# Kernel optimization log

Measured on AMD Instinct MI355X. Metric: run time of the kernel, lower is better.

The kernel has to match this reference:

```python
import jax, jax.numpy as jnp
import numpy as np

B, N, D = 8, 1024, 1024
H, HD = 16, 64          # n_heads, head_dim = D // H
FF = 2 * D              # SwiGLU hidden dim (ffn_dim_mult=2)
EPS = 1e-5


def setup_inputs() -> dict:
    key = jax.random.key(0)
    ks = jax.random.split(key, 10)
    s = 0.02
    return {
        "x": jax.random.normal(ks[0], (B, N, D), dtype=jnp.float32),
        "attn_norm_scale": jnp.ones((D,), jnp.float32),
        "ffn_norm_scale": jnp.ones((D,), jnp.float32),
        "wq": jax.random.normal(ks[1], (D, D), jnp.float32) * s,
        "bq": jnp.zeros((D,), jnp.float32),
        "wk": jax.random.normal(ks[2], (D, D), jnp.float32) * s,
        "bk": jnp.zeros((D,), jnp.float32),
        "wv": jax.random.normal(ks[3], (D, D), jnp.float32) * s,
        "bv": jnp.zeros((D,), jnp.float32),
        "wo": jax.random.normal(ks[4], (D, D), jnp.float32) * s,
        "bo": jnp.zeros((D,), jnp.float32),
        "w_uv": jax.random.normal(ks[5], (D, 2 * FF), jnp.float32) * s,
        "w_out": jax.random.normal(ks[6], (FF, D), jnp.float32) * s,
    }


def _rmsnorm(x, scale):
    xf = x.astype(jnp.float32)
    y = xf * jax.lax.rsqrt(jnp.mean(xf * xf, axis=-1, keepdims=True) + EPS)
    return scale * y.astype(x.dtype)


def reference(x, attn_norm_scale, ffn_norm_scale, wq, bq, wk, bk, wv, bv,
              wo, bo, w_uv, w_out):
    # FFT2D: fft over channel dim then token dim, keep real part
    x = jnp.fft.fft(jnp.fft.fft(x, axis=-1), axis=-2).real.astype(jnp.float32)

    # --- self attention with pre-RMSNorm and residual ---
    xn = _rmsnorm(x, attn_norm_scale)
    q = (xn @ wq + bq).reshape(B, N, H, HD)
    k = (xn @ wk + bk).reshape(B, N, H, HD)
    v = (xn @ wv + bv).reshape(B, N, H, HD)
    scores = jnp.einsum('bnhd,bmhd->bhnm', q, k) / np.sqrt(HD).astype(np.float32)
    attn = jax.nn.softmax(scores, axis=-1)
    o = jnp.einsum('bhnm,bmhd->bnhd', attn, v).reshape(B, N, D)
    x = (o @ wo + bo) + x

    # --- SwiGLU FFN with pre-RMSNorm and residual ---
    xn = _rmsnorm(x, ffn_norm_scale)
    uv = xn @ w_uv                      # [B, N, 2*FF]
    u, vg = uv[..., :FF], uv[..., FF:]
    x = (jax.nn.silu(u) * vg) @ w_out + x
    return x
```

## Files before the change

kernel.cpp:

```cpp
#include <hip/hip_runtime.h>
#include <stdint.h>

typedef unsigned short u16;
typedef __attribute__((ext_vector_type(8))) __bf16 bf16x8;
typedef __attribute__((ext_vector_type(4))) float f32x4;
typedef __attribute__((ext_vector_type(8))) u16 u16x8;

static __device__ __forceinline__ u16 f2bf(float f){
  uint32_t x = __builtin_bit_cast(uint32_t, f);
  x = (x + 0x7FFFu + ((x >> 16) & 1u)) >> 16;
  return (u16)x;
}
static __device__ __forceinline__ u16 f2bf_fast(float f){
  uint32_t x = __builtin_bit_cast(uint32_t, f);
  return (u16)((x + 0x8000u) >> 16);
}
static __device__ __forceinline__ float bf2f(u16 h){
  uint32_t x = ((uint32_t)h) << 16;
  return __builtin_bit_cast(float, x);
}
static __device__ __forceinline__ f32x4 mfma16(bf16x8 a, bf16x8 b, f32x4 c){
  return __builtin_amdgcn_mfma_f32_16x16x32_bf16(a, b, c, 0, 0, 0);
}
static __device__ __forceinline__ void gload16(const void* g, void* l){
  __builtin_amdgcn_global_load_lds(
      (const __attribute__((address_space(1))) void*)(uintptr_t)g,
      (__attribute__((address_space(3))) void*)(uint32_t)(uintptr_t)l,
      16, 0, 0);
}

__global__ __launch_bounds__(256) void k_prep(
    const float* __restrict__ x,  const float* __restrict__ wq,
    const float* __restrict__ wk, const float* __restrict__ wv,
    const float* __restrict__ wo, const float* __restrict__ wuv,
    const float* __restrict__ wout,
    const float* __restrict__ bq, const float* __restrict__ bk,
    const float* __restrict__ bv,
    u16* __restrict__ Cb, u16* __restrict__ Sb, u16* __restrict__ xbt,
    u16* __restrict__ wqkvt, u16* __restrict__ wot, u16* __restrict__ wuvt,
    u16* __restrict__ woutt, float* __restrict__ bqkv)
{
  int bid = blockIdx.x;
  int t = threadIdx.x;
  if (bid < 1024){
    int n = bid, m0 = t * 4;
    #pragma unroll
    for (int i = 0; i < 4; ++i){
      int m = m0 + i;
      int ph = (n * m) & 1023;
      float a = (float)ph * (1.0f / 512.0f);
      int idx = n * 1024 + m;
      Cb[idx] = f2bf(cospif(a)); Sb[idx] = f2bf(sinpif(a));
    }
    return;
  }
  bid -= 1024;
  if (bid >= 18432){
    int i = (bid - 18432) * 256 + t;
    bqkv[i] = i < 1024 ? bq[i] : (i < 2048 ? bk[i - 1024] : bv[i - 2048]);
    return;
  }
  __shared__ float tl[32][33];
  const float* in; u16* out; int Cc, R, bx, by;
  int64_t inOff = 0, outOff = 0;
  bool uvperm = false;
  if (bid < 8192){
    int z = bid >> 10, tile = bid & 1023;
    in = x; out = xbt; Cc = 1024; R = 1024;
    inOff = (int64_t)z << 20; outOff = (int64_t)z << 20;
    bx = tile & 31; by = tile >> 5;
  } else if (bid < 12288){
    int j = (bid - 8192) >> 10, tile = (bid - 8192) & 1023;
    const float* srcs[4] = {wq, wk, wv, wo};
    in = srcs[j]; Cc = 1024; R = 1024;
    if (j < 3){ out = wqkvt; outOff = (int64_t)j << 20; }
    else      { out = wot; }
    bx = tile & 31; by = tile >> 5;
  } else if (bid < 16384){
    int tile = bid - 12288;
    in = wuv; out = wuvt; Cc = 4096; R = 1024; uvperm = true;
    bx = tile & 127; by = tile >> 7;
  } else {
    int tile = bid - 16384;
    in = wout; out = woutt; Cc = 1024; R = 2048;
    bx = tile & 31; by = tile >> 6;
    by = tile >> 5;
  }
  int tc = bx * 32, tr = by * 32;
  int lx = t & 31, ly = t >> 5;
  const float* ip = in + inOff;
  #pragma unroll
  for (int i = 0; i < 32; i += 8)
    tl[ly + i][lx] = ip[(int64_t)(tr + ly + i) * Cc + tc + lx];
  __syncthreads();
  if (uvperm){
    #pragma unroll
    for (int i = 0; i < 32; i += 8){
      int c = tc + ly + i;
      int pr = (c < 2048) ? ((c >> 4) * 32 + (c & 15))
                          : (((c - 2048) >> 4) * 32 + 16 + ((c - 2048) & 15));
      out[(int64_t)pr * 1024 + tr + lx] = f2bf(tl[lx][ly + i]);
    }
  } else {
    u16* op = out + outOff;
    #pragma unroll
    for (int i = 0; i < 32; i += 8)
      op[(int64_t)(tc + ly + i) * R + tr + lx] = f2bf(tl[lx][ly + i]);
  }
}

__global__ __launch_bounds__(256) void k_rmsnorm(const float* __restrict__ x,
                                                 const float* __restrict__ sc,
                                                 u16* __restrict__ out){
  int r = blockIdx.x;
  const float4* px = (const float4*)(x + (int64_t)r * 1024);
  float4 v = px[threadIdx.x];
  float ss = v.x*v.x + v.y*v.y + v.z*v.z + v.w*v.w;
  #pragma unroll
  for (int o = 1; o < 64; o <<= 1) ss += __shfl_xor(ss, o);
  __shared__ float red[4];
  if ((threadIdx.x & 63) == 0) red[threadIdx.x >> 6] = ss;
  __syncthreads();
  float tot = red[0] + red[1] + red[2] + red[3];
  float rs = rsqrtf(tot * (1.0f / 1024.0f) + 1e-5f);
  float4 s4 = ((const float4*)sc)[threadIdx.x];
  ushort4 ov;
  ov.x = f2bf(v.x * rs * s4.x); ov.y = f2bf(v.y * rs * s4.y);
  ov.z = f2bf(v.z * rs * s4.z); ov.w = f2bf(v.w * rs * s4.w);
  ((ushort4*)(out + (int64_t)r * 1024))[threadIdx.x] = ov;
}

__global__ __launch_bounds__(256) void k_fftfin(const u16* __restrict__ Uw,
                                                const float* __restrict__ sc,
                                                float* __restrict__ Y,
                                                u16* __restrict__ xn){
  int row = blockIdx.x;
  int b = row >> 10, k = row & 1023;
  int kp = (k <= 512) ? k : 1024 - k;
  float sgn = (k <= 512) ? -1.0f : 1.0f;
  const u16* ub = Uw + (int64_t)b * (1280 * 1024) + (int64_t)kp * 1024;
  const u16* wb = ub + 640 * 1024;
  int c4 = threadIdx.x * 4;
  ushort4 uu = *(const ushort4*)(ub + c4);
  ushort4 ww = *(const ushort4*)(wb + c4);
  float y0 = bf2f(uu.x) + sgn * bf2f(ww.x);
  float y1 = bf2f(uu.y) + sgn * bf2f(ww.y);
  float y2 = bf2f(uu.z) + sgn * bf2f(ww.z);
  float y3 = bf2f(uu.w) + sgn * bf2f(ww.w);
  float ss = y0*y0 + y1*y1 + y2*y2 + y3*y3;
  #pragma unroll
  for (int o = 1; o < 64; o <<= 1) ss += __shfl_xor(ss, o);
  __shared__ float red[4];
  if ((threadIdx.x & 63) == 0) red[threadIdx.x >> 6] = ss;
  __syncthreads();
  float tot = red[0] + red[1] + red[2] + red[3];
  float rs = rsqrtf(tot * (1.0f / 1024.0f) + 1e-5f);
  float4 s4 = ((const float4*)sc)[threadIdx.x];
  float4 yo; yo.x = y0; yo.y = y1; yo.z = y2; yo.w = y3;
  ((float4*)(Y + (int64_t)row * 1024))[threadIdx.x] = yo;
  ushort4 ov;
  ov.x = f2bf(y0 * rs * s4.x); ov.y = f2bf(y1 * rs * s4.y);
  ov.z = f2bf(y2 * rs * s4.z); ov.w = f2bf(y3 * rs * s4.w);
  ((ushort4*)(xn + (int64_t)row * 1024))[threadIdx.x] = ov;
}

template<bool SILU>
__global__ __launch_bounds__(256, 4) void k_gemm4(
    const u16* __restrict__ A0, const u16* __restrict__ A1,
    const u16* __restrict__ B0, const u16* __restrict__ B1,
    void* Cout, const float* __restrict__ bias, const float* resid,
    int nkt, int rowSplit, int lda, int ldb, int ldc,
    int64_t aB, int64_t bB, int64_t cB, int outBf16)
{
  __shared__ char smem[32768];

  int z = blockIdx.z;
  int nwg = gridDim.x * gridDim.y;
  int bid = blockIdx.y * gridDim.x + blockIdx.x;
  int sw = (bid & 7) * (nwg >> 3) + (bid >> 3);
  int bx = sw % gridDim.x, by = sw / gridDim.x;

  int tm = by * 128, tn = bx * 128;
  int tid = threadIdx.x;
  int lane = tid & 63, w = tid >> 6;
  int lr = lane & 15, lg = lane >> 4;
  int wOffM = (w >> 1) * 64, wOffN = (w & 1) * 64;

  const u16* Ap = ((tm < rowSplit) ? A0 : A1) + (int64_t)z * aB;
  const u16* Bp = ((tm < rowSplit) ? B0 : B1) + (int64_t)z * bB;
  int64_t cOff = (int64_t)z * cB;

  int r0_, kg0_, r1_, kg1_;
  {
    int D = tid * 16, line = D >> 7, sp = ((D >> 4) & 7) ^ (line & 7);
    r0_ = line * 2 + (sp >> 2); kg0_ = sp & 3;
    D = tid * 16 + 4096; line = D >> 7; sp = ((D >> 4) & 7) ^ (line & 7);
    r1_ = line * 2 + (sp >> 2); kg1_ = sp & 3;
  }
  const u16* pA0 = Ap + (int64_t)(tm + r0_) * lda + kg0_ * 8;
  const u16* pA1 = Ap + (int64_t)(tm + r1_) * lda + kg1_ * 8;
  const u16* pB0 = Bp + (int64_t)(tn + r0_) * ldb + kg0_ * 8;
  const u16* pB1 = Bp + (int64_t)(tn + r1_) * ldb + kg1_ * 8;

  int slotR = (lg + ((lr & 1) << 2)) ^ ((lr >> 1) & 7);
  int aRB = ((wOffM >> 1) + (lr >> 1)) * 128 + slotR * 16;
  int bRB = ((wOffN >> 1) + (lr >> 1)) * 128 + slotR * 16;

  const f32x4 fz = {0.f, 0.f, 0.f, 0.f};
  f32x4 acc[4][4];
  #pragma unroll
  for (int i = 0; i < 4; ++i)
    #pragma unroll
    for (int j = 0; j < 4; ++j) acc[i][j] = fz;

  auto STAGE = [&](int kt, int bf){
    int k0 = kt * 32;
    char* d = smem + bf * 16384 + tid * 16;
    gload16(pA0 + k0, d);
    gload16(pA1 + k0, d + 4096);
    gload16(pB0 + k0, d + 8192);
    gload16(pB1 + k0, d + 12288);
  };
  auto COMPUTE = [&](const char* Ab){
    const char* Bb = Ab + 8192;
    bf16x8 af[4], bfr[4];
    #pragma unroll
    for (int i = 0; i < 4; ++i) af[i]  = *(const bf16x8*)(Ab + aRB + i * 1024);
    #pragma unroll
    for (int j = 0; j < 4; ++j) bfr[j] = *(const bf16x8*)(Bb + bRB + j * 1024);
    #pragma unroll
    for (int i = 0; i < 4; ++i)
      #pragma unroll
      for (int j = 0; j < 4; ++j)
        acc[i][j] = mfma16(af[i], bfr[j], acc[i][j]);
  };

  STAGE(0, 0);
  __syncthreads();
  for (int kt = 0; kt < nkt; kt += 2){
    STAGE(kt + 1, 1);
    COMPUTE(smem);
    __syncthreads();
    if (kt + 2 < nkt) STAGE(kt + 2, 0);
    COMPUTE(smem + 16384);
    __syncthreads();
  }

  if constexpr (SILU){
    int colBase = ((tn + wOffN) >> 1) + lr;
    #pragma unroll
    for (int i = 0; i < 4; ++i){
      #pragma unroll
      for (int jj = 0; jj < 4; ++jj){
        int row = tm + wOffM + i * 16 + lg * 4 + jj;
        #pragma unroll
        for (int jp = 0; jp < 2; ++jp){
          float u = acc[i][jp * 2][jj], v = acc[i][jp * 2 + 1][jj];
          float s = u / (1.0f + __expf(-u));
          ((u16*)Cout)[(int64_t)row * ldc + colBase + jp * 16] = f2bf(s * v);
        }
      }
    }
  } else {
    #pragma unroll
    for (int i = 0; i < 4; ++i){
      #pragma unroll
      for (int j = 0; j < 4; ++j){
        int col = tn + wOffN + j * 16 + lr;
        float badd = bias ? bias[col] : 0.0f;
        #pragma unroll
        for (int jj = 0; jj < 4; ++jj){
          int row = tm + wOffM + i * 16 + lg * 4 + jj;
          int64_t idx = cOff + (int64_t)row * ldc + col;
          float v = acc[i][j][jj] + badd;
          if (resid) v += resid[idx];
          if (outBf16) ((u16*)Cout)[idx] = f2bf(v);
          else         ((float*)Cout)[idx] = v;
        }
      }
    }
  }
}

__global__ __launch_bounds__(256) void k_vtrans(const u16* __restrict__ qkv,
                                                u16* __restrict__ vt){
  __shared__ u16 T[64 * 65];
  int bh = blockIdx.y; int b = bh >> 4, h = bh & 15;
  int kt = blockIdx.x;
  int t = threadIdx.x;
  const u16* src = qkv + (int64_t)(b * 1024 + kt * 64) * 3072 + 2048 + h * 64;
  #pragma unroll
  for (int i = 0; i < 16; ++i){
    int idx = i * 256 + t;
    int r = idx >> 6, c = idx & 63;
    T[r * 65 + c] = src[(int64_t)r * 3072 + c];
  }
  __syncthreads();
  u16* dst = vt + (int64_t)bh * 65536 + kt * 64;
  #pragma unroll
  for (int i = 0; i < 16; ++i){
    int idx = i * 256 + t;
    int dr = idx >> 6, kc = idx & 63;
    dst[(int64_t)dr * 1024 + kc] = T[kc * 65 + dr];
  }
}

__global__ __launch_bounds__(512, 4) void k_attn2(const u16* __restrict__ qkv,
                                                  const u16* __restrict__ vt,
                                                  u16* __restrict__ O){
  __shared__ u16 Ks[2][4096];
  __shared__ u16 Vts[2][4096];
  __shared__ u16 Pl[8][2304];
  int bh = blockIdx.y; int b = bh >> 4, h = bh & 15;
  int qt = blockIdx.x;
  int t = threadIdx.x, w = t >> 6, lane = t & 63, lr = lane & 15, lg = lane >> 4;
  int sr = t >> 3, sl = t & 7;
  int swz = (sl ^ (sr & 7)) * 8;

  const u16* kg = qkv + (int64_t)b * 1024 * 3072 + 1024 + h * 64;
  const u16* vg = vt + (int64_t)bh * 65536;

  const u16* qrow = qkv + (int64_t)(b * 1024 + qt * 256 + w * 32 + lr) * 3072 + h * 64;
  bf16x8 aq[2][2];
  #pragma unroll
  for (int m = 0; m < 2; ++m)
    #pragma unroll
    for (int kc = 0; kc < 2; ++kc)
      aq[m][kc] = *(const bf16x8*)(qrow + (int64_t)m * 16 * 3072 + kc * 32 + lg * 8);

  const f32x4 fz = {0.f, 0.f, 0.f, 0.f};
  f32x4 o_[2][4];
  float lj[2][4];
  #pragma unroll
  for (int m = 0; m < 2; ++m){
    #pragma unroll
    for (int d = 0; d < 4; ++d) o_[m][d] = fz;
    #pragma unroll
    for (int j = 0; j < 4; ++j) lj[m][j] = 0.f;
  }

  #define STAGE(ktile, bn) do {                                                   \
    gload16(kg + (int64_t)((ktile) * 64 + sr) * 3072 + swz,                       \
            (char*)Ks + (bn) * 8192 + t * 16);                                    \
    gload16(vg + (int64_t)sr * 1024 + (ktile) * 64 + swz,                         \
            (char*)Vts + (bn) * 8192 + t * 16);                                   \
  } while (0)

  STAGE(0, 0);
  __syncthreads();
  int buf = 0;
  int lsw = lr & 7;

  const float CSC = 0.1803368801111204f;
  const float MSH = 8.656170245333781f;

  #pragma unroll 1
  for (int kt = 0; kt < 16; ++kt){
    if (kt < 15) STAGE(kt + 1, buf ^ 1);

    f32x4 s[2][4];
    #pragma unroll
    for (int m = 0; m < 2; ++m)
      #pragma unroll
      for (int n = 0; n < 4; ++n) s[m][n] = fz;
    #pragma unroll
    for (int n = 0; n < 4; ++n){
      #pragma unroll
      for (int kc = 0; kc < 2; ++kc){
        bf16x8 kb = *(const bf16x8*)&Ks[buf][(n * 16 + lr) * 64 + (((kc * 4 + lg) ^ lsw) * 8)];
        s[0][n] = mfma16(aq[0][kc], kb, s[0][n]);
        s[1][n] = mfma16(aq[1][kc], kb, s[1][n]);
      }
    }

    #pragma unroll
    for (int m = 0; m < 2; ++m){
      #pragma unroll
      for (int j = 0; j < 4; ++j){
        float p0 = exp2f(fmaf(s[m][0][j], CSC, -MSH));
        float p1 = exp2f(fmaf(s[m][1][j], CSC, -MSH));
        float p2 = exp2f(fmaf(s[m][2][j], CSC, -MSH));
        float p3 = exp2f(fmaf(s[m][3][j], CSC, -MSH));
        lj[m][j] += (p0 + p1) + (p2 + p3);
        u16* pb = &Pl[w][(m * 16 + lg * 4 + j) * 72 + lr];
        pb[0]  = f2bf_fast(p0); pb[16] = f2bf_fast(p1);
        pb[32] = f2bf_fast(p2); pb[48] = f2bf_fast(p3);
      }
    }
    asm volatile("s_waitcnt lgkmcnt(0)" ::: "memory");
    __builtin_amdgcn_sched_barrier(0);

    #pragma unroll
    for (int kc = 0; kc < 2; ++kc){
      bf16x8 pa0 = *(const bf16x8*)&Pl[w][(lr) * 72 + kc * 32 + lg * 8];
      bf16x8 pa1 = *(const bf16x8*)&Pl[w][(16 + lr) * 72 + kc * 32 + lg * 8];
      #pragma unroll
      for (int dt = 0; dt < 4; ++dt){
        bf16x8 vb = *(const bf16x8*)&Vts[buf][(dt * 16 + lr) * 64 + (((kc * 4 + lg) ^ lsw) * 8)];
        o_[0][dt] = mfma16(pa0, vb, o_[0][dt]);
        o_[1][dt] = mfma16(pa1, vb, o_[1][dt]);
      }
    }
    __syncthreads();
    buf ^= 1;
  }
  #undef STAGE

  u16* obase = O + (int64_t)(b * 1024 + qt * 256 + w * 32) * 1024 + h * 64;
  #pragma unroll
  for (int m = 0; m < 2; ++m){
    #pragma unroll
    for (int j = 0; j < 4; ++j){
      float l = lj[m][j];
      l += __shfl_xor(l, 1); l += __shfl_xor(l, 2);
      l += __shfl_xor(l, 4); l += __shfl_xor(l, 8);
      float inv = 1.0f / l;
      int q = m * 16 + lg * 4 + j;
      #pragma unroll
      for (int dt = 0; dt < 4; ++dt)
        obase[(int64_t)q * 1024 + dt * 16 + lr] = f2bf(o_[m][dt][j] * inv);
    }
  }
}

extern "C" void kernel_launch(void* const* d_in, const int* in_sizes, int n_in,
                              void* d_out, int out_size, void* d_ws, size_t ws_size,
                              hipStream_t stream)
{
  (void)in_sizes; (void)n_in; (void)out_size; (void)ws_size;
  const float* x    = (const float*)d_in[0];
  const float* ans  = (const float*)d_in[1];
  const float* fns  = (const float*)d_in[2];
  const float* wq   = (const float*)d_in[3];
  const float* bq   = (const float*)d_in[4];
  const float* wk   = (const float*)d_in[5];
  const float* bk   = (const float*)d_in[6];
  const float* wv   = (const float*)d_in[7];
  const float* bvv  = (const float*)d_in[8];
  const float* wo   = (const float*)d_in[9];
  const float* bo   = (const float*)d_in[10];
  const float* wuv  = (const float*)d_in[11];
  const float* wout = (const float*)d_in[12];

  char* ws = (char*)d_ws;
  const size_t MB = 1u << 20;
  const int64_t M1 = 1024 * 1024;
  const int64_t FB = (int64_t)1280 * 1024;
  const int BIG = 1 << 30;
  u16*  xbt   = (u16*)(ws + 0 * MB);
  u16*  Xcs   = (u16*)(ws + 16 * MB);
  u16*  Uw    = (u16*)(ws + 36 * MB);
  u16*  xn    = (u16*)(ws + 56 * MB);
  u16*  qkv   = (u16*)(ws + 0 * MB);
  u16*  vtg   = (u16*)(ws + 72 * MB);
  u16*  Obuf  = (u16*)(ws + 88 * MB);
  u16*  xn2   = (u16*)(ws + 0 * MB);
  u16*  g     = (u16*)(ws + 16 * MB);
  u16*  Cb    = (u16*)(ws + 104 * MB);
  u16*  Sb    = (u16*)(ws + 106 * MB);
  u16*  wqkvt = (u16*)(ws + 108 * MB);
  u16*  wot   = (u16*)(ws + 114 * MB);
  u16*  wuvt  = (u16*)(ws + 116 * MB);
  u16*  woutt = (u16*)(ws + 124 * MB);
  float* bqkv = (float*)(ws + 128 * MB);
  float* outF = (float*)d_out;

  k_prep<<<dim3(19468), 256, 0, stream>>>(x, wq, wk, wv, wo, wuv, wout,
      bq, bk, bvv, Cb, Sb, xbt, wqkvt, wot, wuvt, woutt, bqkv);

  k_gemm4<false><<<dim3(8, 10, 8), 256, 0, stream>>>(
      Cb, Sb - 640 * 1024, xbt, xbt, Xcs, nullptr, nullptr,
      32, 640, 1024, 1024, 1024, 0, M1, FB, 1);
  k_gemm4<false><<<dim3(8, 10, 8), 256, 0, stream>>>(
      Xcs, Xcs, Cb, Sb, Uw, nullptr, nullptr,
      32, 640, 1024, 1024, 1024, FB, 0, FB, 1);
  k_fftfin<<<dim3(8192), 256, 0, stream>>>(Uw, ans, outF, xn);

  k_gemm4<false><<<dim3(24, 64, 1), 256, 0, stream>>>(
      xn, xn, wqkvt, wqkvt, qkv, bqkv, nullptr,
      32, BIG, 1024, 1024, 3072, 0, 0, 0, 1);
  k_vtrans<<<dim3(16, 128), 256, 0, stream>>>(qkv, vtg);
  k_attn2<<<dim3(4, 128), 512, 0, stream>>>(qkv, vtg, Obuf);
  k_gemm4<false><<<dim3(8, 64, 1), 256, 0, stream>>>(
      Obuf, Obuf, wot, wot, d_out, bo, outF,
      32, BIG, 1024, 1024, 1024, 0, 0, 0, 0);

  k_rmsnorm<<<dim3(8192), 256, 0, stream>>>(outF, fns, xn2);
  k_gemm4<true><<<dim3(32, 64, 1), 256, 0, stream>>>(
      xn2, xn2, wuvt, wuvt, g, nullptr, nullptr,
      32, BIG, 1024, 1024, 2048, 0, 0, 0, 1);
  k_gemm4<false><<<dim3(8, 64, 1), 256, 0, stream>>>(
      g, g, woutt, woutt, d_out, nullptr, outF,
      64, BIG, 2048, 2048, 1024, 0, 0, 0, 0);
}
```

Measured before the change: 422.3 us.

## Switch GEMM to 32x32x16 MFMA and fuse V transpose into QKV epilogue

Rewrites the shared GEMM kernel to use 32x32x16 bf16 MFMA with 2x2 accumulator tiles per wave in place of 4x4 tiles of 16x16x32. The LDS read addressing and the SwiGLU weight permutation are changed to match the new output layout. The QKV GEMM now writes V already transposed into the vt buffer, so the separate k_vtrans kernel and its extra pass over V are removed. This cuts LDS fragment reads and one launch, but changes the epilogue store patterns and may alter register pressure.

```diff
diff --git a/kernel.cpp b/kernel.cpp
--- a/kernel.cpp
+++ b/kernel.cpp
@@ -4,6 +4,7 @@
 typedef unsigned short u16;
 typedef __attribute__((ext_vector_type(8))) __bf16 bf16x8;
 typedef __attribute__((ext_vector_type(4))) float f32x4;
+typedef __attribute__((ext_vector_type(16))) float f32x16;
 typedef __attribute__((ext_vector_type(8))) u16 u16x8;
 
 static __device__ __forceinline__ u16 f2bf(float f){
@@ -21,6 +22,9 @@
 }
 static __device__ __forceinline__ f32x4 mfma16(bf16x8 a, bf16x8 b, f32x4 c){
   return __builtin_amdgcn_mfma_f32_16x16x32_bf16(a, b, c, 0, 0, 0);
+}
+static __device__ __forceinline__ f32x16 mfma32(bf16x8 a, bf16x8 b, f32x16 c){
+  return __builtin_amdgcn_mfma_f32_32x32x16_bf16(a, b, c, 0, 0, 0);
 }
 static __device__ __forceinline__ void gload16(const void* g, void* l){
   __builtin_amdgcn_global_load_lds(
@@ -83,8 +87,7 @@
   } else {
     int tile = bid - 16384;
     in = wout; out = woutt; Cc = 1024; R = 2048;
-    bx = tile & 31; by = tile >> 6;
-    by = tile >> 5;
+    bx = tile & 31; by = tile >> 5;
   }
   int tc = bx * 32, tr = by * 32;
   int lx = t & 31, ly = t >> 5;
@@ -97,8 +100,8 @@
     #pragma unroll
     for (int i = 0; i < 32; i += 8){
       int c = tc + ly + i;
-      int pr = (c < 2048) ? ((c >> 4) * 32 + (c & 15))
-                          : (((c - 2048) >> 4) * 32 + 16 + ((c - 2048) & 15));
+      int pr = (c < 2048) ? ((c >> 5) * 64 + (c & 31))
+                          : (((c - 2048) >> 5) * 64 + 32 + ((c - 2048) & 31));
       out[(int64_t)pr * 1024 + tr + lx] = f2bf(tl[lx][ly + i]);
     }
   } else {
@@ -165,10 +168,11 @@
 }
 
 template<bool SILU>
-__global__ __launch_bounds__(256, 4) void k_gemm4(
+__global__ __launch_bounds__(256, 4) void k_gemm5(
     const u16* __restrict__ A0, const u16* __restrict__ A1,
     const u16* __restrict__ B0, const u16* __restrict__ B1,
     void* Cout, const float* __restrict__ bias, const float* resid,
+    u16* __restrict__ vtbuf, int vtn0,
     int nkt, int rowSplit, int lda, int ldb, int ldc,
     int64_t aB, int64_t bB, int64_t cB, int outBf16)
 {
@@ -183,7 +187,7 @@
   int tm = by * 128, tn = bx * 128;
   int tid = threadIdx.x;
   int lane = tid & 63, w = tid >> 6;
-  int lr = lane & 15, lg = lane >> 4;
+  int la31 = lane & 31, lhi = lane >> 5;
   int wOffM = (w >> 1) * 64, wOffN = (w & 1) * 64;
 
   const u16* Ap = ((tm < rowSplit) ? A0 : A1) + (int64_t)z * aB;
@@ -202,16 +206,14 @@
   const u16* pB0 = Bp + (int64_t)(tn + r0_) * ldb + kg0_ * 8;
   const u16* pB1 = Bp + (int64_t)(tn + r1_) * ldb + kg1_ * 8;
 
-  int slotR = (lg + ((lr & 1) << 2)) ^ ((lr >> 1) & 7);
-  int aRB = ((wOffM >> 1) + (lr >> 1)) * 128 + slotR * 16;
-  int bRB = ((wOffN >> 1) + (lr >> 1)) * 128 + slotR * 16;
-
-  const f32x4 fz = {0.f, 0.f, 0.f, 0.f};
-  f32x4 acc[4][4];
-  #pragma unroll
-  for (int i = 0; i < 4; ++i)
-    #pragma unroll
-    for (int j = 0; j < 4; ++j) acc[i][j] = fz;
+  int lineA = (wOffM + la31) >> 1;
+  int aRB = lineA * 128 + (((lhi + ((la31 & 1) << 2)) ^ (lineA & 7)) << 4);
+  int lineB = (wOffN + la31) >> 1;
+  int bRB = lineB * 128 + (((lhi + ((la31 & 1) << 2)) ^ (lineB & 7)) << 4);
+
+  const f32x16 fz = {0.f,0.f,0.f,0.f,0.f,0.f,0.f,0.f,0.f,0.f,0.f,0.f,0.f,0.f,0.f,0.f};
+  f32x16 acc[2][2];
+  acc[0][0] = fz; acc[0][1] = fz; acc[1][0] = fz; acc[1][1] = fz;
 
   auto STAGE = [&](int kt, int bf){
     int k0 = kt * 32;
@@ -223,16 +225,24 @@
   };
   auto COMPUTE = [&](const char* Ab){
     const char* Bb = Ab + 8192;
-    bf16x8 af[4], bfr[4];
-    #pragma unroll
-    for (int i = 0; i < 4; ++i) af[i]  = *(const bf16x8*)(Ab + aRB + i * 1024);
-    #pragma unroll
-    for (int j = 0; j < 4; ++j) bfr[j] = *(const bf16x8*)(Bb + bRB + j * 1024);
-    #pragma unroll
-    for (int i = 0; i < 4; ++i)
-      #pragma unroll
-      for (int j = 0; j < 4; ++j)
-        acc[i][j] = mfma16(af[i], bfr[j], acc[i][j]);
+    bf16x8 a[2][2], b[2][2];
+    #pragma unroll
+    for (int m = 0; m < 2; ++m)
+      #pragma unroll
+      for (int kc = 0; kc < 2; ++kc)
+        a[m][kc] = *(const bf16x8*)(Ab + ((aRB + m * 2048) ^ (kc << 5)));
+    #pragma unroll
+    for (int n = 0; n < 2; ++n)
+      #pragma unroll
+      for (int kc = 0; kc < 2; ++kc)
+        b[n][kc] = *(const bf16x8*)(Bb + ((bRB + n * 2048) ^ (kc << 5)));
+    #pragma unroll
+    for (int m = 0; m < 2; ++m)
+      #pragma unroll
+      for (int n = 0; n < 2; ++n){
+        acc[m][n] = mfma32(a[m][0], b[n][0], acc[m][n]);
+        acc[m][n] = mfma32(a[m][1], b[n][1], acc[m][n]);
+      }
   };
 
   STAGE(0, 0);
@@ -247,61 +257,62 @@
   }
 
   if constexpr (SILU){
-    int colBase = ((tn + wOffN) >> 1) + lr;
-    #pragma unroll
-    for (int i = 0; i < 4; ++i){
-      #pragma unroll
-      for (int jj = 0; jj < 4; ++jj){
-        int row = tm + wOffM + i * 16 + lg * 4 + jj;
+    int colBase = ((tn + wOffN) >> 1) + la31;
+    #pragma unroll
+    for (int m = 0; m < 2; ++m){
+      #pragma unroll
+      for (int q = 0; q < 4; ++q){
         #pragma unroll
-        for (int jp = 0; jp < 2; ++jp){
-          float u = acc[i][jp * 2][jj], v = acc[i][jp * 2 + 1][jj];
+        for (int j = 0; j < 4; ++j){
+          int row = tm + wOffM + m * 32 + j + 8 * q + 4 * lhi;
+          float u = acc[m][0][q * 4 + j], v = acc[m][1][q * 4 + j];
           float s = u / (1.0f + __expf(-u));
-          ((u16*)Cout)[(int64_t)row * ldc + colBase + jp * 16] = f2bf(s * v);
+          ((u16*)Cout)[(int64_t)row * ldc + colBase] = f2bf(s * v);
         }
       }
     }
-  } else {
-    #pragma unroll
-    for (int i = 0; i < 4; ++i){
-      #pragma unroll
-      for (int j = 0; j < 4; ++j){
-        int col = tn + wOffN + j * 16 + lr;
+    return;
+  }
+  if (vtbuf && tn >= vtn0){
+    int b = tm >> 10;
+    #pragma unroll
+    for (int m = 0; m < 2; ++m){
+      #pragma unroll
+      for (int n = 0; n < 2; ++n){
+        int col = tn + wOffN + n * 32 + la31;
+        int hv = (col - 2048) >> 6, d = (col - 2048) & 63;
         float badd = bias ? bias[col] : 0.0f;
+        u16* vb = vtbuf + ((int64_t)(b * 16 + hv) << 16) + d * 1024;
+        int key0 = (tm & 1023) + wOffM + m * 32 + 4 * lhi;
         #pragma unroll
-        for (int jj = 0; jj < 4; ++jj){
-          int row = tm + wOffM + i * 16 + lg * 4 + jj;
-          int64_t idx = cOff + (int64_t)row * ldc + col;
-          float v = acc[i][j][jj] + badd;
-          if (resid) v += resid[idx];
-          if (outBf16) ((u16*)Cout)[idx] = f2bf(v);
-          else         ((float*)Cout)[idx] = v;
+        for (int q = 0; q < 4; ++q){
+          ushort4 pk;
+          pk.x = f2bf(acc[m][n][q * 4 + 0] + badd);
+          pk.y = f2bf(acc[m][n][q * 4 + 1] + badd);
+          pk.z = f2bf(acc[m][n][q * 4 + 2] + badd);
+          pk.w = f2bf(acc[m][n][q * 4 + 3] + badd);
+          *(ushort4*)(vb + key0 + 8 * q) = pk;
         }
       }
     }
-  }
-}
-
-__global__ __launch_bounds__(256) void k_vtrans(const u16* __restrict__ qkv,
-                                                u16* __restrict__ vt){
-  __shared__ u16 T[64 * 65];
-  int bh = blockIdx.y; int b = bh >> 4, h = bh & 15;
-  int kt = blockIdx.x;
-  int t = threadIdx.x;
-  const u16* src = qkv + (int64_t)(b * 1024 + kt * 64) * 3072 + 2048 + h * 64;
-  #pragma unroll
-  for (int i = 0; i < 16; ++i){
-    int idx = i * 256 + t;
-    int r = idx >> 6, c = idx & 63;
-    T[r * 65 + c] = src[(int64_t)r * 3072 + c];
-  }
-  __syncthreads();
-  u16* dst = vt + (int64_t)bh * 65536 + kt * 64;
-  #pragma unroll
-  for (int i = 0; i < 16; ++i){
-    int idx = i * 256 + t;
-    int dr = idx >> 6, kc = idx & 63;
-    dst[(int64_t)dr * 1024 + kc] = T[kc * 65 + dr];
+    return;
+  }
+  #pragma unroll
+  for (int m = 0; m < 2; ++m){
+    #pragma unroll
+    for (int n = 0; n < 2; ++n){
+      int col = tn + wOffN + n * 32 + la31;
+      float badd = bias ? bias[col] : 0.0f;
+      #pragma unroll
+      for (int r = 0; r < 16; ++r){
+        int row = tm + wOffM + m * 32 + (r & 3) + 8 * (r >> 2) + 4 * lhi;
+        int64_t idx = cOff + (int64_t)row * ldc + col;
+        float v = acc[m][n][r] + badd;
+        if (resid) v += resid[idx];
+        if (outBf16) ((u16*)Cout)[idx] = f2bf(v);
+        else         ((float*)Cout)[idx] = v;
+      }
+    }
   }
 }
 
@@ -468,28 +479,27 @@
   k_prep<<<dim3(19468), 256, 0, stream>>>(x, wq, wk, wv, wo, wuv, wout,
       bq, bk, bvv, Cb, Sb, xbt, wqkvt, wot, wuvt, woutt, bqkv);
 
-  k_gemm4<false><<<dim3(8, 10, 8), 256, 0, stream>>>(
-      Cb, Sb - 640 * 1024, xbt, xbt, Xcs, nullptr, nullptr,
+  k_gemm5<false><<<dim3(8, 10, 8), 256, 0, stream>>>(
+      Cb, Sb - 640 * 1024, xbt, xbt, Xcs, nullptr, nullptr, nullptr, BIG,
       32, 640, 1024, 1024, 1024, 0, M1, FB, 1);
-  k_gemm4<false><<<dim3(8, 10, 8), 256, 0, stream>>>(
-      Xcs, Xcs, Cb, Sb, Uw, nullptr, nullptr,
+  k_gemm5<false><<<dim3(8, 10, 8), 256, 0, stream>>>(
+      Xcs, Xcs, Cb, Sb, Uw, nullptr, nullptr, nullptr, BIG,
       32, 640, 1024, 1024, 1024, FB, 0, FB, 1);
   k_fftfin<<<dim3(8192), 256, 0, stream>>>(Uw, ans, outF, xn);
 
-  k_gemm4<false><<<dim3(24, 64, 1), 256, 0, stream>>>(
-      xn, xn, wqkvt, wqkvt, qkv, bqkv, nullptr,
+  k_gemm5<false><<<dim3(24, 64, 1), 256, 0, stream>>>(
+      xn, xn, wqkvt, wqkvt, qkv, bqkv, nullptr, vtg, 2048,
       32, BIG, 1024, 1024, 3072, 0, 0, 0, 1);
-  k_vtrans<<<dim3(16, 128), 256, 0, stream>>>(qkv, vtg);
   k_attn2<<<dim3(4, 128), 512, 0, stream>>>(qkv, vtg, Obuf);
-  k_gemm4<false><<<dim3(8, 64, 1), 256, 0, stream>>>(
-      Obuf, Obuf, wot, wot, d_out, bo, outF,
+  k_gemm5<false><<<dim3(8, 64, 1), 256, 0, stream>>>(
+      Obuf, Obuf, wot, wot, d_out, bo, outF, nullptr, BIG,
       32, BIG, 1024, 1024, 1024, 0, 0, 0, 0);
 
   k_rmsnorm<<<dim3(8192), 256, 0, stream>>>(outF, fns, xn2);
-  k_gemm4<true><<<dim3(32, 64, 1), 256, 0, stream>>>(
-      xn2, xn2, wuvt, wuvt, g, nullptr, nullptr,
+  k_gemm5<true><<<dim3(32, 64, 1), 256, 0, stream>>>(
+      xn2, xn2, wuvt, wuvt, g, nullptr, nullptr, nullptr, BIG,
       32, BIG, 1024, 1024, 2048, 0, 0, 0, 1);
-  k_gemm4<false><<<dim3(8, 64, 1), 256, 0, stream>>>(
-      g, g, woutt, woutt, d_out, nullptr, outF,
+  k_gemm5<false><<<dim3(8, 64, 1), 256, 0, stream>>>(
+      g, g, woutt, woutt, d_out, nullptr, outF, nullptr, BIG,
       64, BIG, 2048, 2048, 1024, 0, 0, 0, 0);
 }
```

Measured after the change: 470.9 us. 1.12x slower.

## Exploit Hermitian symmetry on channel axis to shrink second DFT GEMM

Applied to the files above, without the earlier changes.

The second FFT GEMM now computes only 640 output columns (k<=512 plus padding) per batch instead of 1024. The finalize kernel reconstructs the remaining columns from conjugate symmetry, flipping the sign of the imaginary-product term. This cuts that GEMM's work and Uw traffic, at the cost of gathered, non-vectorized loads in k_fftfin. The GEMM tile swizzle also now handles grid counts not divisible by 8 and gains an optional column-major tile order used by the first DFT GEMM. A redundant index assignment in k_prep is cleaned up as well.

```diff
diff --git a/kernel.cpp b/kernel.cpp
--- a/kernel.cpp
+++ b/kernel.cpp
@@ -83,8 +83,7 @@
   } else {
     int tile = bid - 16384;
     in = wout; out = woutt; Cc = 1024; R = 2048;
-    bx = tile & 31; by = tile >> 6;
-    by = tile >> 5;
+    bx = tile & 31; by = tile >> 5;
   }
   int tc = bx * 32, tr = by * 32;
   int lx = t & 31, ly = t >> 5;
@@ -137,17 +136,19 @@
   int row = blockIdx.x;
   int b = row >> 10, k = row & 1023;
   int kp = (k <= 512) ? k : 1024 - k;
-  float sgn = (k <= 512) ? -1.0f : 1.0f;
-  const u16* ub = Uw + (int64_t)b * (1280 * 1024) + (int64_t)kp * 1024;
-  const u16* wb = ub + 640 * 1024;
-  int c4 = threadIdx.x * 4;
-  ushort4 uu = *(const ushort4*)(ub + c4);
-  ushort4 ww = *(const ushort4*)(wb + c4);
-  float y0 = bf2f(uu.x) + sgn * bf2f(ww.x);
-  float y1 = bf2f(uu.y) + sgn * bf2f(ww.y);
-  float y2 = bf2f(uu.z) + sgn * bf2f(ww.z);
-  float y3 = bf2f(uu.w) + sgn * bf2f(ww.w);
-  float ss = y0*y0 + y1*y1 + y2*y2 + y3*y3;
+  float sm = (k <= 512) ? 1.0f : -1.0f;
+  const u16* ub = Uw + (int64_t)b * 819200 + (int64_t)kp * 640;
+  const u16* wb = ub + 640 * 640;
+  int c0 = threadIdx.x * 4;
+  float y[4];
+  #pragma unroll
+  for (int i = 0; i < 4; ++i){
+    int c = c0 + i;
+    int tp = (c <= 512) ? c : 1024 - c;
+    float st = (c <= 512) ? sm : -sm;
+    y[i] = bf2f(ub[tp]) - st * bf2f(wb[tp]);
+  }
+  float ss = y[0]*y[0] + y[1]*y[1] + y[2]*y[2] + y[3]*y[3];
   #pragma unroll
   for (int o = 1; o < 64; o <<= 1) ss += __shfl_xor(ss, o);
   __shared__ float red[4];
@@ -156,15 +157,15 @@
   float tot = red[0] + red[1] + red[2] + red[3];
   float rs = rsqrtf(tot * (1.0f / 1024.0f) + 1e-5f);
   float4 s4 = ((const float4*)sc)[threadIdx.x];
-  float4 yo; yo.x = y0; yo.y = y1; yo.z = y2; yo.w = y3;
+  float4 yo; yo.x = y[0]; yo.y = y[1]; yo.z = y[2]; yo.w = y[3];
   ((float4*)(Y + (int64_t)row * 1024))[threadIdx.x] = yo;
   ushort4 ov;
-  ov.x = f2bf(y0 * rs * s4.x); ov.y = f2bf(y1 * rs * s4.y);
-  ov.z = f2bf(y2 * rs * s4.z); ov.w = f2bf(y3 * rs * s4.w);
+  ov.x = f2bf(y[0] * rs * s4.x); ov.y = f2bf(y[1] * rs * s4.y);
+  ov.z = f2bf(y[2] * rs * s4.z); ov.w = f2bf(y[3] * rs * s4.w);
   ((ushort4*)(xn + (int64_t)row * 1024))[threadIdx.x] = ov;
 }
 
-template<bool SILU>
+template<bool SILU, bool COLCHUNK>
 __global__ __launch_bounds__(256, 4) void k_gemm4(
     const u16* __restrict__ A0, const u16* __restrict__ A1,
     const u16* __restrict__ B0, const u16* __restrict__ B1,
@@ -177,8 +178,11 @@
   int z = blockIdx.z;
   int nwg = gridDim.x * gridDim.y;
   int bid = blockIdx.y * gridDim.x + blockIdx.x;
-  int sw = (bid & 7) * (nwg >> 3) + (bid >> 3);
-  int bx = sw % gridDim.x, by = sw / gridDim.x;
+  int q = nwg >> 3, r = nwg & 7, xc = bid & 7, off = bid >> 3;
+  int sw = (xc < r ? xc * (q + 1) : r * (q + 1) + (xc - r) * q) + off;
+  int bx, by;
+  if (COLCHUNK){ bx = sw / gridDim.y; by = sw % gridDim.y; }
+  else         { bx = sw % gridDim.x; by = sw / gridDim.x; }
 
   int tm = by * 128, tn = bx * 128;
   int tid = threadIdx.x;
@@ -446,6 +450,7 @@
   const size_t MB = 1u << 20;
   const int64_t M1 = 1024 * 1024;
   const int64_t FB = (int64_t)1280 * 1024;
+  const int64_t FB2 = (int64_t)1280 * 640;
   const int BIG = 1 << 30;
   u16*  xbt   = (u16*)(ws + 0 * MB);
   u16*  Xcs   = (u16*)(ws + 16 * MB);
@@ -468,28 +473,28 @@
   k_prep<<<dim3(19468), 256, 0, stream>>>(x, wq, wk, wv, wo, wuv, wout,
       bq, bk, bvv, Cb, Sb, xbt, wqkvt, wot, wuvt, woutt, bqkv);
 
-  k_gemm4<false><<<dim3(8, 10, 8), 256, 0, stream>>>(
+  k_gemm4<false, true><<<dim3(8, 10, 8), 256, 0, stream>>>(
       Cb, Sb - 640 * 1024, xbt, xbt, Xcs, nullptr, nullptr,
       32, 640, 1024, 1024, 1024, 0, M1, FB, 1);
-  k_gemm4<false><<<dim3(8, 10, 8), 256, 0, stream>>>(
+  k_gemm4<false, false><<<dim3(5, 10, 8), 256, 0, stream>>>(
       Xcs, Xcs, Cb, Sb, Uw, nullptr, nullptr,
-      32, 640, 1024, 1024, 1024, FB, 0, FB, 1);
+      32, 640, 1024, 1024, 640, FB, 0, FB2, 1);
   k_fftfin<<<dim3(8192), 256, 0, stream>>>(Uw, ans, outF, xn);
 
-  k_gemm4<false><<<dim3(24, 64, 1), 256, 0, stream>>>(
+  k_gemm4<false, false><<<dim3(24, 64, 1), 256, 0, stream>>>(
       xn, xn, wqkvt, wqkvt, qkv, bqkv, nullptr,
       32, BIG, 1024, 1024, 3072, 0, 0, 0, 1);
   k_vtrans<<<dim3(16, 128), 256, 0, stream>>>(qkv, vtg);
   k_attn2<<<dim3(4, 128), 512, 0, stream>>>(qkv, vtg, Obuf);
-  k_gemm4<false><<<dim3(8, 64, 1), 256, 0, stream>>>(
+  k_gemm4<false, false><<<dim3(8, 64, 1), 256, 0, stream>>>(
       Obuf, Obuf, wot, wot, d_out, bo, outF,
       32, BIG, 1024, 1024, 1024, 0, 0, 0, 0);
 
   k_rmsnorm<<<dim3(8192), 256, 0, stream>>>(outF, fns, xn2);
-  k_gemm4<true><<<dim3(32, 64, 1), 256, 0, stream>>>(
+  k_gemm4<true, false><<<dim3(32, 64, 1), 256, 0, stream>>>(
       xn2, xn2, wuvt, wuvt, g, nullptr, nullptr,
       32, BIG, 1024, 1024, 2048, 0, 0, 0, 1);
-  k_gemm4<false><<<dim3(8, 64, 1), 256, 0, stream>>>(
+  k_gemm4<false, false><<<dim3(8, 64, 1), 256, 0, stream>>>(
       g, g, woutt, woutt, d_out, nullptr, outF,
       64, BIG, 2048, 2048, 1024, 0, 0, 0, 0);
 }
```

Result: faster. 411.4 us (-2.6%).
